# Optimization experiments

Hardware: AMD Instinct MI355X
Metric: run time of the kernel (lower is better)

The kernel has to match this reference:

```python
import jax, jax.numpy as jnp
import numpy as np

# ---- Cl(4,1) Cayley table (conformal GA: metric +,+,+,+,-) ----
_METRIC = (1.0, 1.0, 1.0, 1.0, -1.0)

def _reorder_sign(a, b):
    # sign from counting swaps to bring blade product to canonical order
    a >>= 1
    s = 0
    while a:
        s += bin(a & b).count("1")
        a >>= 1
    return -1.0 if (s & 1) else 1.0

def _build_cayley():
    C = np.zeros((32, 32, 32), dtype=np.float32)
    for a in range(32):
        for b in range(32):
            s = _reorder_sign(a, b)
            common = a & b
            for i in range(5):
                if (common >> i) & 1:
                    s *= _METRIC[i]
            C[a, b, a ^ b] += s
    return C

CAYLEY = _build_cayley()  # [32,32,32]; out_k = sum_ij C[i,j,k] x_i y_j

EPS = 1e-8

def normalize_cl41(x):
    n = jnp.sqrt(jnp.sum(x * x, axis=-1, keepdims=True))
    return x / (n + EPS)


def setup_inputs() -> dict:
    key = jax.random.key(0)
    k_x, k_wi, k_bi, k_wo, k_bo = jax.random.split(key, 5)
    B, S, D, H = 64, 2048, 6, 8
    x = jax.random.normal(k_x, (B, S, D), dtype=jnp.float32)
    W_in = jax.random.normal(k_wi, (D, H * 32), dtype=jnp.float32) * (1.0 / np.sqrt(D))
    b_in = jax.random.normal(k_bi, (H * 32,), dtype=jnp.float32) * 0.01
    W_out = jax.random.normal(k_wo, (H * 32, 32), dtype=jnp.float32) * (1.0 / np.sqrt(H * 32))
    b_out = jax.random.normal(k_bo, (32,), dtype=jnp.float32) * 0.01
    return {"x": x, "W_in": W_in, "b_in": b_in, "W_out": W_out, "b_out": b_out}


def reference(x, W_in, b_in, W_out, b_out):
    B, S, D = x.shape
    H = W_in.shape[1] // 32
    C = jnp.asarray(CAYLEY)
    # project inputs to per-channel multivectors: (B,S,H,32)
    u = (x @ W_in + b_in).reshape(B, S, H, 32)
    # initial rotor state: identity (scalar blade = 1)
    psi0 = jnp.zeros((B, H, 32), dtype=x.dtype).at[..., 0].set(1.0)

    def step(psi, u_t):  # u_t: (B,H,32)
        delta = normalize_cl41(u_t.at[..., 0].add(1.0))
        psi = normalize_cl41(jnp.einsum("bhi,bhj,ijk->bhk", delta, psi, C))
        return psi, psi

    _, psi_seq = jax.lax.scan(step, psi0, jnp.swapaxes(u, 0, 1))  # (S,B,H,32)
    out = normalize_cl41(psi_seq.reshape(S, B, H * 32) @ W_out + b_out)  # (S,B,32)
    return jnp.swapaxes(out, 0, 1)  # (B,S,32)
```

## Files before the change

kernel.cpp:

```cpp
#include <hip/hip_runtime.h>
#include <hip/hip_bf16.h>
#include <stdint.h>

#define BB 64
#define SS 2048
#define DD 6
#define HH 8
#define NCH 512
#define CHUNKS 256
#define LCH 8

typedef unsigned short ushort_t;
typedef __attribute__((ext_vector_type(8))) __bf16 bf16x8;
typedef __attribute__((ext_vector_type(4))) float f32x4;

struct SignTab { float s[32][32]; };

constexpr int popc5_c(unsigned v) {
    int c = 0;
    for (int i = 0; i < 5; ++i) c += (v >> i) & 1u;
    return c;
}

constexpr SignTab make_signs() {
    SignTab t{};
    for (int a = 0; a < 32; ++a) {
        for (int b = 0; b < 32; ++b) {
            int cnt = 0;
            unsigned aa = ((unsigned)a) >> 1;
            while (aa) { cnt += popc5_c(aa & (unsigned)b); aa >>= 1; }
            if ((a & b) & 16) cnt += 1;
            t.s[a][b] = (cnt & 1) ? -1.0f : 1.0f;
        }
    }
    return t;
}

constexpr SignTab SGN = make_signs();

__device__ __forceinline__ void gp_cl41(const float* __restrict__ a,
                                        const float* __restrict__ b,
                                        float* __restrict__ o) {
#pragma unroll
    for (int k = 0; k < 32; ++k) o[k] = 0.0f;
#pragma unroll
    for (int i = 0; i < 32; ++i) {
#pragma unroll
        for (int k = 0; k < 32; ++k) {
            o[k] = fmaf(SGN.s[i][i ^ k] * a[i], b[i ^ k], o[k]);
        }
    }
}

__device__ __forceinline__ float sumsq32(const float* v) {
    float n0 = 0.f, n1 = 0.f, n2 = 0.f, n3 = 0.f;
#pragma unroll
    for (int k = 0; k < 32; k += 4) {
        n0 = fmaf(v[k+0], v[k+0], n0);
        n1 = fmaf(v[k+1], v[k+1], n1);
        n2 = fmaf(v[k+2], v[k+2], n2);
        n3 = fmaf(v[k+3], v[k+3], n3);
    }
    return (n0 + n1) + (n2 + n3);
}

__device__ __forceinline__ float rsq(float n) {
    return __builtin_amdgcn_rsqf(n);
}

__device__ __forceinline__ uint32_t f2bf_rne(float f) {
    uint32_t u = __float_as_uint(f);
    return (u + 0x7FFFu + ((u >> 16) & 1u)) >> 16;
}

__device__ __forceinline__ void make_delta(const float4* __restrict__ sW,
                                           const float* __restrict__ x6,
                                           float* __restrict__ dl) {
#pragma unroll
    for (int j4 = 0; j4 < 8; ++j4) {
        float4 bv = sW[48 + j4];
        dl[4*j4+0] = bv.x; dl[4*j4+1] = bv.y; dl[4*j4+2] = bv.z; dl[4*j4+3] = bv.w;
    }
#pragma unroll
    for (int d = 0; d < 6; ++d) {
        float a = x6[d];
#pragma unroll
        for (int j4 = 0; j4 < 8; ++j4) {
            float4 w = sW[d * 8 + j4];
            dl[4*j4+0] = fmaf(a, w.x, dl[4*j4+0]);
            dl[4*j4+1] = fmaf(a, w.y, dl[4*j4+1]);
            dl[4*j4+2] = fmaf(a, w.z, dl[4*j4+2]);
            dl[4*j4+3] = fmaf(a, w.w, dl[4*j4+3]);
        }
    }
    dl[0] += 1.0f;
}

__global__ __launch_bounds__(256, 1) void k_scan(
        const float* __restrict__ x, const float* __restrict__ W_in,
        const float* __restrict__ b_in, float* __restrict__ Ebuf) {
    __shared__ float4 sW4[57];
    __shared__ float sT[CHUNKS][36];

    int chain = blockIdx.x;
    int b = chain >> 3, h = chain & 7;
    int c = threadIdx.x;

    if (c < 56) {
        float4 v;
        if (c < 48) {
            int d = c / 8, j4 = c % 8;
            const float* p = W_in + d * 256 + h * 32 + 4 * j4;
            v = make_float4(p[0], p[1], p[2], p[3]);
        } else {
            const float* p = b_in + h * 32 + 4 * (c - 48);
            v = make_float4(p[0], p[1], p[2], p[3]);
        }
        sW4[c] = v;
    }
    __syncthreads();

    const float* xrow = x + ((size_t)b * SS + (size_t)c * LCH) * DD;

    float P[32], O[32], dl[32];

    {
        float xv[12];
        const float4* xp = (const float4*)xrow;
#pragma unroll
        for (int m = 0; m < 3; ++m) {
            float4 t4 = xp[m];
            xv[4*m] = t4.x; xv[4*m+1] = t4.y; xv[4*m+2] = t4.z; xv[4*m+3] = t4.w;
        }
        make_delta(sW4, xv, O);
        make_delta(sW4, xv + 6, dl);
        gp_cl41(dl, O, P);
    }
#pragma unroll 1
    for (int pr = 1; pr < 4; ++pr) {
        float xv[12];
        const float4* xp = (const float4*)(xrow + 12 * pr);
#pragma unroll
        for (int m = 0; m < 3; ++m) {
            float4 t4 = xp[m];
            xv[4*m] = t4.x; xv[4*m+1] = t4.y; xv[4*m+2] = t4.z; xv[4*m+3] = t4.w;
        }
        make_delta(sW4, xv, dl);
        gp_cl41(dl, P, O);
        make_delta(sW4, xv + 6, dl);
        gp_cl41(dl, O, P);
    }

    float v[32];
    {
        float inv = rsq(sumsq32(P));
#pragma unroll
        for (int k = 0; k < 32; ++k) v[k] = P[k] * inv;
#pragma unroll
        for (int m = 0; m < 8; ++m)
            *(float4*)&sT[c][4*m] = make_float4(v[4*m], v[4*m+1], v[4*m+2], v[4*m+3]);
    }
    __syncthreads();

#pragma unroll 1
    for (int off = 1; off < CHUNKS; off <<= 1) {
        bool act = (c >= off);
        if (act) {
#pragma unroll
            for (int m = 0; m < 8; ++m) {
                float4 t4 = *(const float4*)&sT[c - off][4*m];
                O[4*m] = t4.x; O[4*m+1] = t4.y; O[4*m+2] = t4.z; O[4*m+3] = t4.w;
            }
        }
        __syncthreads();
        if (act) {
            gp_cl41(v, O, P);
            float inv = rsq(sumsq32(P));
#pragma unroll
            for (int k = 0; k < 32; ++k) v[k] = P[k] * inv;
#pragma unroll
            for (int m = 0; m < 8; ++m)
                *(float4*)&sT[c][4*m] = make_float4(v[4*m], v[4*m+1], v[4*m+2], v[4*m+3]);
        }
        __syncthreads();
    }

    float* dst = Ebuf + (size_t)chain * CHUNKS * 32;
    if (c == 0) {
        *(float4*)dst = make_float4(1.f, 0.f, 0.f, 0.f);
#pragma unroll
        for (int m = 1; m < 8; ++m) *(float4*)(dst + 4*m) = make_float4(0.f, 0.f, 0.f, 0.f);
    }
    if (c < CHUNKS - 1) {
        float* d2 = dst + (size_t)(c + 1) * 32;
#pragma unroll
        for (int m = 0; m < 8; ++m)
            *(float4*)(d2 + 4*m) = make_float4(v[4*m], v[4*m+1], v[4*m+2], v[4*m+3]);
    }
}

__global__ __launch_bounds__(64, 2) void k_chain_proj(
        const float* __restrict__ x, const float* __restrict__ W_in,
        const float* __restrict__ b_in, const float* __restrict__ Ebuf,
        const float* __restrict__ W_out, const float* __restrict__ b_out,
        float* __restrict__ out) {
    __shared__ float4 sW4[8][57];
    __shared__ float sX[384];
    __shared__ ushort_t psiT[16][264];

    int task = blockIdx.x;
    int b = task >> 5, grp = task & 31;
    int c0 = grp * 8;
    int lane = threadIdx.x;
    int cl = lane >> 3, h = lane & 7;
    int q = lane >> 4, n0 = lane & 15;

    for (int idx = lane; idx < 448; idx += 64) {
        int hh = idx / 56, r = idx % 56;
        float4 v;
        if (r < 48) {
            int d = r / 8, j4 = r % 8;
            const float* p = W_in + d * 256 + hh * 32 + 4 * j4;
            v = make_float4(p[0], p[1], p[2], p[3]);
        } else {
            const float* p = b_in + hh * 32 + 4 * (r - 48);
            v = make_float4(p[0], p[1], p[2], p[3]);
        }
        sW4[hh][r] = v;
    }

    {
        const float2* xp = (const float2*)(x + ((size_t)b * SS + (size_t)c0 * LCH) * DD);
        float2* sx2 = (float2*)sX;
#pragma unroll
        for (int m = 0; m < 3; ++m) sx2[lane * 3 + m] = xp[lane * 3 + m];
    }

    float p[32];
    {
        const float4* ep = (const float4*)(Ebuf +
                (((size_t)b * HH + h) * CHUNKS + (c0 + cl)) * 32);
#pragma unroll
        for (int m = 0; m < 8; ++m) {
            float4 t4 = ep[m];
            p[4*m] = t4.x; p[4*m+1] = t4.y; p[4*m+2] = t4.z; p[4*m+3] = t4.w;
        }
    }

    bf16x8 Bf[2][8];
#pragma unroll
    for (int nt = 0; nt < 2; ++nt)
#pragma unroll
        for (int kk = 0; kk < 8; ++kk) {
            union { ushort_t u[8]; bf16x8 v; } tmp;
#pragma unroll
            for (int j = 0; j < 8; ++j)
                tmp.u[j] = (ushort_t)f2bf_rne(W_out[(kk * 32 + q * 8 + j) * 32 + nt * 16 + n0]);
            Bf[nt][kk] = tmp.v;
        }
    float bn0 = b_out[n0], bn1 = b_out[16 + n0];

    __syncthreads();

#pragma unroll 1
    for (int pr = 0; pr < 4; ++pr) {
        float x0[6], x1[6];
#pragma unroll
        for (int d = 0; d < 6; ++d) {
            x0[d] = sX[(cl * 8 + 2 * pr) * 6 + d];
            x1[d] = sX[(cl * 8 + 2 * pr + 1) * 6 + d];
        }

        float dl[32], o[32];
        make_delta(sW4[h], x0, dl);
        gp_cl41(dl, p, o);
        {
            float inv = rsq(sumsq32(o));
            uint32_t pk[16];
#pragma unroll
            for (int m = 0; m < 16; ++m)
                pk[m] = f2bf_rne(o[2*m] * inv) | (f2bf_rne(o[2*m+1] * inv) << 16);
            uint4* dst = (uint4*)&psiT[cl * 2][h * 32];
#pragma unroll
            for (int m = 0; m < 4; ++m)
                dst[m] = make_uint4(pk[4*m], pk[4*m+1], pk[4*m+2], pk[4*m+3]);
        }
        make_delta(sW4[h], x1, dl);
        gp_cl41(dl, o, p);
        {
            float inv = rsq(sumsq32(p));
            uint32_t pk[16];
#pragma unroll
            for (int m = 0; m < 16; ++m)
                pk[m] = f2bf_rne(p[2*m] * inv) | (f2bf_rne(p[2*m+1] * inv) << 16);
            uint4* dst = (uint4*)&psiT[cl * 2 + 1][h * 32];
#pragma unroll
            for (int m = 0; m < 4; ++m)
                dst[m] = make_uint4(pk[4*m], pk[4*m+1], pk[4*m+2], pk[4*m+3]);
        }

        __syncthreads();

        f32x4 acc0 = {0.f, 0.f, 0.f, 0.f};
        f32x4 acc1 = {0.f, 0.f, 0.f, 0.f};
#pragma unroll
        for (int kk = 0; kk < 8; ++kk) {
            bf16x8 af = *(const bf16x8*)&psiT[n0][kk * 32 + q * 8];
            acc0 = __builtin_amdgcn_mfma_f32_16x16x32_bf16(af, Bf[0][kk], acc0, 0, 0, 0);
            acc1 = __builtin_amdgcn_mfma_f32_16x16x32_bf16(af, Bf[1][kk], acc1, 0, 0, 0);
        }

        float c0v[4], c1v[4], ssq[4];
#pragma unroll
        for (int i = 0; i < 4; ++i) {
            c0v[i] = acc0[i] + bn0;
            c1v[i] = acc1[i] + bn1;
            ssq[i] = c0v[i] * c0v[i] + c1v[i] * c1v[i];
        }
#pragma unroll
        for (int m = 1; m < 16; m <<= 1) {
#pragma unroll
            for (int i = 0; i < 4; ++i) ssq[i] += __shfl_xor(ssq[i], m);
        }
#pragma unroll
        for (int i = 0; i < 4; ++i) {
            float inv = rsq(ssq[i]);
            int mrow = q * 4 + i;
            int s = (c0 + (mrow >> 1)) * LCH + 2 * pr + (mrow & 1);
            size_t row = (size_t)b * SS + s;
            out[row * 32 + n0]      = c0v[i] * inv;
            out[row * 32 + 16 + n0] = c1v[i] * inv;
        }

        __syncthreads();
    }
}

extern "C" void kernel_launch(void* const* d_in, const int* in_sizes, int n_in,
                              void* d_out, int out_size, void* d_ws, size_t ws_size,
                              hipStream_t stream) {
    const float* x     = (const float*)d_in[0];
    const float* W_in  = (const float*)d_in[1];
    const float* b_in  = (const float*)d_in[2];
    const float* W_out = (const float*)d_in[3];
    const float* b_out = (const float*)d_in[4];
    float* out = (float*)d_out;

    float* Ebuf = (float*)d_ws;

    k_scan      <<<NCH,  256, 0, stream>>>(x, W_in, b_in, Ebuf);
    k_chain_proj<<<2048,  64, 0, stream>>>(x, W_in, b_in, Ebuf, W_out, b_out, out);
}
```

Baseline: 175.2 us.

## Replace Hillis-Steele chunk scan with tree-reduced scan and widen projection blocks

The per-chain chunk scan no longer runs an 8-level Hillis-Steele scan over 256 chunk products. It first combines pairs and quads into a 64-element level, scans that with a single wave over 6 levels, then expands the exclusive prefixes back to all 256 chunks. This cuts geometric products and block barriers. The projection kernel now packs four waves per block, stages W_out once into swizzled bf16 LDS instead of scattered global loads per lane, and uses an XOR-swizzled psiT layout to avoid bank conflicts. make_delta is fused to compute two step deltas at once. In exchange the scan uses more LDS, leaves three waves idle during the 64-wide scan, and changes the order of normalization.

Measured after the change: 192.6 us. 10.0% more time.

```diff
diff --git a/kernel.cpp b/kernel.cpp
--- a/kernel.cpp
+++ b/kernel.cpp
@@ -73,34 +73,68 @@
     return (u + 0x7FFFu + ((u >> 16) & 1u)) >> 16;
 }
 
-__device__ __forceinline__ void make_delta(const float4* __restrict__ sW,
-                                           const float* __restrict__ x6,
-                                           float* __restrict__ dl) {
+__device__ __forceinline__ void loadp(const float4* __restrict__ a, int stride,
+                                      int idx, float* __restrict__ v) {
+#pragma unroll
+    for (int m = 0; m < 8; ++m) {
+        float4 t = a[m * stride + idx];
+        v[4*m] = t.x; v[4*m+1] = t.y; v[4*m+2] = t.z; v[4*m+3] = t.w;
+    }
+}
+__device__ __forceinline__ void storep(float4* __restrict__ a, int stride,
+                                       int idx, const float* __restrict__ v) {
+#pragma unroll
+    for (int m = 0; m < 8; ++m)
+        a[m * stride + idx] = make_float4(v[4*m], v[4*m+1], v[4*m+2], v[4*m+3]);
+}
+
+__device__ __forceinline__ void make_delta2(const float4* __restrict__ sW,
+                                            const float* __restrict__ xv,
+                                            float* __restrict__ dl0,
+                                            float* __restrict__ dl1) {
 #pragma unroll
     for (int j4 = 0; j4 < 8; ++j4) {
         float4 bv = sW[48 + j4];
-        dl[4*j4+0] = bv.x; dl[4*j4+1] = bv.y; dl[4*j4+2] = bv.z; dl[4*j4+3] = bv.w;
+        dl0[4*j4+0] = bv.x; dl0[4*j4+1] = bv.y; dl0[4*j4+2] = bv.z; dl0[4*j4+3] = bv.w;
+        dl1[4*j4+0] = bv.x; dl1[4*j4+1] = bv.y; dl1[4*j4+2] = bv.z; dl1[4*j4+3] = bv.w;
     }
 #pragma unroll
     for (int d = 0; d < 6; ++d) {
-        float a = x6[d];
+        float a0 = xv[d], a1 = xv[6 + d];
 #pragma unroll
         for (int j4 = 0; j4 < 8; ++j4) {
             float4 w = sW[d * 8 + j4];
-            dl[4*j4+0] = fmaf(a, w.x, dl[4*j4+0]);
-            dl[4*j4+1] = fmaf(a, w.y, dl[4*j4+1]);
-            dl[4*j4+2] = fmaf(a, w.z, dl[4*j4+2]);
-            dl[4*j4+3] = fmaf(a, w.w, dl[4*j4+3]);
-        }
-    }
-    dl[0] += 1.0f;
+            dl0[4*j4+0] = fmaf(a0, w.x, dl0[4*j4+0]);
+            dl0[4*j4+1] = fmaf(a0, w.y, dl0[4*j4+1]);
+            dl0[4*j4+2] = fmaf(a0, w.z, dl0[4*j4+2]);
+            dl0[4*j4+3] = fmaf(a0, w.w, dl0[4*j4+3]);
+            dl1[4*j4+0] = fmaf(a1, w.x, dl1[4*j4+0]);
+            dl1[4*j4+1] = fmaf(a1, w.y, dl1[4*j4+1]);
+            dl1[4*j4+2] = fmaf(a1, w.z, dl1[4*j4+2]);
+            dl1[4*j4+3] = fmaf(a1, w.w, dl1[4*j4+3]);
+        }
+    }
+    dl0[0] += 1.0f;
+    dl1[0] += 1.0f;
+}
+
+__device__ __forceinline__ void loadx12(const float* __restrict__ xr, float* __restrict__ xv) {
+    const float4* xp = (const float4*)xr;
+#pragma unroll
+    for (int m = 0; m < 3; ++m) {
+        float4 t4 = xp[m];
+        xv[4*m] = t4.x; xv[4*m+1] = t4.y; xv[4*m+2] = t4.z; xv[4*m+3] = t4.w;
+    }
 }
 
 __global__ __launch_bounds__(256, 1) void k_scan(
         const float* __restrict__ x, const float* __restrict__ W_in,
         const float* __restrict__ b_in, float* __restrict__ Ebuf) {
     __shared__ float4 sW4[57];
-    __shared__ float sT[CHUNKS][36];
+    __shared__ float4 sTv[8 * CHUNKS];
+    __shared__ float4 sUv[8 * 128];
+    __shared__ float4 sGv[8 * 64];
+    __shared__ float4 sPv[8 * 64];
 
     int chain = blockIdx.x;
     int b = chain >> 3, h = chain & 7;
@@ -121,101 +155,132 @@
     __syncthreads();
 
     const float* xrow = x + ((size_t)b * SS + (size_t)c * LCH) * DD;
-
-    float P[32], O[32], dl[32];
-
+    float P[32], O[32];
     {
         float xv[12];
-        const float4* xp = (const float4*)xrow;
-#pragma unroll
-        for (int m = 0; m < 3; ++m) {
-            float4 t4 = xp[m];
-            xv[4*m] = t4.x; xv[4*m+1] = t4.y; xv[4*m+2] = t4.z; xv[4*m+3] = t4.w;
-        }
-        make_delta(sW4, xv, O);
-        make_delta(sW4, xv + 6, dl);
-        gp_cl41(dl, O, P);
+        loadx12(xrow, xv);
+        float dl0[32], dl1[32];
+        make_delta2(sW4, xv, dl0, dl1);
+        gp_cl41(dl1, dl0, P);
     }
 #pragma unroll 1
     for (int pr = 1; pr < 4; ++pr) {
         float xv[12];
-        const float4* xp = (const float4*)(xrow + 12 * pr);
-#pragma unroll
-        for (int m = 0; m < 3; ++m) {
-            float4 t4 = xp[m];
-            xv[4*m] = t4.x; xv[4*m+1] = t4.y; xv[4*m+2] = t4.z; xv[4*m+3] = t4.w;
-        }
-        make_delta(sW4, xv, dl);
-        gp_cl41(dl, P, O);
-        make_delta(sW4, xv + 6, dl);
-        gp_cl41(dl, O, P);
-    }
-
-    float v[32];
+        loadx12(xrow + 12 * pr, xv);
+        float dl0[32], dl1[32];
+        make_delta2(sW4, xv, dl0, dl1);
+        gp_cl41(dl0, P, O);
+        gp_cl41(dl1, O, P);
+    }
     {
         float inv = rsq(sumsq32(P));
 #pragma unroll
-        for (int k = 0; k < 32; ++k) v[k] = P[k] * inv;
+        for (int k = 0; k < 32; ++k) P[k] *= inv;
+        storep(sTv, CHUNKS, c, P);
+    }
+    __syncthreads();
+
+    int wave = c >> 6, lane = c & 63;
+    int w_act = (blockIdx.x ^ (blockIdx.x >> 8)) & 3;
+
+    if (c < 128) {
+        float A_[32], B_[32], U_[32];
+        loadp(sTv, CHUNKS, 2 * c + 1, A_);
+        loadp(sTv, CHUNKS, 2 * c,     B_);
+        gp_cl41(A_, B_, U_);
+        storep(sUv, 128, c, U_);
+    }
+    __syncthreads();
+
+    if (wave == w_act) {
+        float A_[32], B_[32], G_[32];
+        loadp(sUv, 128, 2 * lane + 1, A_);
+        loadp(sUv, 128, 2 * lane,     B_);
+        gp_cl41(A_, B_, G_);
+        storep(sGv, 64, lane, G_);
+    } else if (wave == (w_act ^ 2)) {
+        float A_[32], B_[32], P3_[32];
+        loadp(sTv, CHUNKS, 4 * lane + 2, A_);
+        loadp(sUv, 128, 2 * lane, B_);
+        gp_cl41(A_, B_, P3_);
+        storep(sPv, 64, lane, P3_);
+    }
+    __syncthreads();
+
+    {
+        bool act = (wave == w_act);
+        float gv[32];
+        if (act) loadp(sGv, 64, lane, gv);
+#pragma unroll 1
+        for (int off = 1; off < 64; off <<= 1) {
+            if (act && lane >= off) {
+                float w_[32], o_[32];
+                loadp(sGv, 64, lane - off, w_);
+                gp_cl41(gv, w_, o_);
+                float inv = rsq(sumsq32(o_));
+#pragma unroll
+                for (int k = 0; k < 32; ++k) gv[k] = o_[k] * inv;
+                storep(sGv, 64, lane, gv);
+            }
+            __syncthreads();
+        }
+    }
+
+    {
+        int g = c >> 2, r = c & 3;
+        float EG[32], E_[32];
+        if (g == 0) {
+#pragma unroll
+            for (int k = 0; k < 32; ++k) EG[k] = (k == 0) ? 1.f : 0.f;
+        } else {
+            loadp(sGv, 64, g - 1, EG);
+        }
+        if (r == 0) {
+#pragma unroll
+            for (int k = 0; k < 32; ++k) E_[k] = EG[k];
+        } else {
+            float L[32];
+            if (r == 1)      loadp(sTv, CHUNKS, c - 1, L);
+            else if (r == 2) loadp(sUv, 128, (c - 2) >> 1, L);
+            else             loadp(sPv, 64, g, L);
+            gp_cl41(L, EG, E_);
+        }
+        float inv = rsq(sumsq32(E_));
+        float4* dst = (float4*)(Ebuf + ((size_t)chain * CHUNKS + c) * 32);
 #pragma unroll
         for (int m = 0; m < 8; ++m)
-            *(float4*)&sT[c][4*m] = make_float4(v[4*m], v[4*m+1], v[4*m+2], v[4*m+3]);
-    }
-    __syncthreads();
-
-#pragma unroll 1
-    for (int off = 1; off < CHUNKS; off <<= 1) {
-        bool act = (c >= off);
-        if (act) {
-#pragma unroll
-            for (int m = 0; m < 8; ++m) {
-                float4 t4 = *(const float4*)&sT[c - off][4*m];
-                O[4*m] = t4.x; O[4*m+1] = t4.y; O[4*m+2] = t4.z; O[4*m+3] = t4.w;
-            }
-        }
-        __syncthreads();
-        if (act) {
-            gp_cl41(v, O, P);
-            float inv = rsq(sumsq32(P));
-#pragma unroll
-            for (int k = 0; k < 32; ++k) v[k] = P[k] * inv;
-#pragma unroll
-            for (int m = 0; m < 8; ++m)
-                *(float4*)&sT[c][4*m] = make_float4(v[4*m], v[4*m+1], v[4*m+2], v[4*m+3]);
-        }
-        __syncthreads();
-    }
-
-    float* dst = Ebuf + (size_t)chain * CHUNKS * 32;
-    if (c == 0) {
-        *(float4*)dst = make_float4(1.f, 0.f, 0.f, 0.f);
-#pragma unroll
-        for (int m = 1; m < 8; ++m) *(float4*)(dst + 4*m) = make_float4(0.f, 0.f, 0.f, 0.f);
-    }
-    if (c < CHUNKS - 1) {
-        float* d2 = dst + (size_t)(c + 1) * 32;
-#pragma unroll
-        for (int m = 0; m < 8; ++m)
-            *(float4*)(d2 + 4*m) = make_float4(v[4*m], v[4*m+1], v[4*m+2], v[4*m+3]);
-    }
-}
-
-__global__ __launch_bounds__(64, 2) void k_chain_proj(
+            dst[m] = make_float4(E_[4*m] * inv, E_[4*m+1] * inv,
+                                 E_[4*m+2] * inv, E_[4*m+3] * inv);
+    }
+}
+
+__global__ __launch_bounds__(256, 1) void k_chain_proj(
         const float* __restrict__ x, const float* __restrict__ W_in,
         const float* __restrict__ b_in, const float* __restrict__ Ebuf,
         const float* __restrict__ W_out, const float* __restrict__ b_out,
         float* __restrict__ out) {
     __shared__ float4 sW4[8][57];
-    __shared__ float sX[384];
-    __shared__ ushort_t psiT[16][264];
-
-    int task = blockIdx.x;
-    int b = task >> 5, grp = task & 31;
+    __shared__ float sX[1536];
+    __shared__ ushort_t Wt[32 * 256];
+    __shared__ ushort_t psiT[4 * 16 * 256];
+
+    int tid = threadIdx.x;
+    int wv = tid >> 6, lane = tid & 63;
+    int b = blockIdx.x >> 3, gq = blockIdx.x & 7;
+    int grp = gq * 4 + wv;
     int c0 = grp * 8;
-    int lane = threadIdx.x;
     int cl = lane >> 3, h = lane & 7;
     int q = lane >> 4, n0 = lane & 15;
 
-    for (int idx = lane; idx < 448; idx += 64) {
+    float4 pv[8];
+    {
+        const float4* ep = (const float4*)(Ebuf +
+                (((size_t)b * HH + h) * CHUNKS + (c0 + cl)) * 32);
+#pragma unroll
+        for (int m = 0; m < 8; ++m) pv[m] = ep[m];
+    }
+
+    for (int idx = tid; idx < 448; idx += 256) {
         int hh = idx / 56, r = idx % 56;
         float4 v;
         if (r < 48) {
@@ -230,84 +295,101 @@
     }
 
     {
-        const float2* xp = (const float2*)(x + ((size_t)b * SS + (size_t)c0 * LCH) * DD);
-        float2* sx2 = (float2*)sX;
-#pragma unroll
-        for (int m = 0; m < 3; ++m) sx2[lane * 3 + m] = xp[lane * 3 + m];
-    }
+        const float4* xp = (const float4*)(x + ((size_t)b * SS + (size_t)gq * 256) * DD);
+        float4* sx4 = (float4*)sX;
+        for (int idx = tid; idx < 384; idx += 256) sx4[idx] = xp[idx];
+    }
+
+    for (int idx = tid; idx < 2048; idx += 256) {
+        int k = idx >> 3, n4 = (idx & 7) << 2;
+        float4 w4 = ((const float4*)W_out)[idx];
+        ushort_t vals[4] = { (ushort_t)f2bf_rne(w4.x), (ushort_t)f2bf_rne(w4.y),
+                             (ushort_t)f2bf_rne(w4.z), (ushort_t)f2bf_rne(w4.w) };
+#pragma unroll
+        for (int j = 0; j < 4; ++j) {
+            int n = n4 + j;
+            uint32_t off = (uint32_t)(n * 512 + 2 * k) ^ (uint32_t)((n & 7) << 4);
+            *(ushort_t*)((char*)Wt + off) = vals[j];
+        }
+    }
+    __syncthreads();
 
     float p[32];
-    {
-        const float4* ep = (const float4*)(Ebuf +
-                (((size_t)b * HH + h) * CHUNKS + (c0 + cl)) * 32);
-#pragma unroll
-        for (int m = 0; m < 8; ++m) {
-            float4 t4 = ep[m];
-            p[4*m] = t4.x; p[4*m+1] = t4.y; p[4*m+2] = t4.z; p[4*m+3] = t4.w;
-        }
+#pragma unroll
+    for (int m = 0; m < 8; ++m) {
+        p[4*m] = pv[m].x; p[4*m+1] = pv[m].y; p[4*m+2] = pv[m].z; p[4*m+3] = pv[m].w;
     }
 
     bf16x8 Bf[2][8];
 #pragma unroll
-    for (int nt = 0; nt < 2; ++nt)
-#pragma unroll
-        for (int kk = 0; kk < 8; ++kk) {
-            union { ushort_t u[8]; bf16x8 v; } tmp;
-#pragma unroll
-            for (int j = 0; j < 8; ++j)
-                tmp.u[j] = (ushort_t)f2bf_rne(W_out[(kk * 32 + q * 8 + j) * 32 + nt * 16 + n0]);
-            Bf[nt][kk] = tmp.v;
-        }
+    for (int nt = 0; nt < 2; ++nt) {
+        int n = nt * 16 + n0;
+        uint32_t rb = (uint32_t)(n * 512);
+        uint32_t sw = (uint32_t)((n & 7) << 4);
+#pragma unroll
+        for (int kk = 0; kk < 8; ++kk)
+            Bf[nt][kk] = *(const bf16x8*)((const char*)Wt + ((rb + kk * 64 + q * 16) ^ sw));
+    }
     float bn0 = b_out[n0], bn1 = b_out[16 + n0];
 
-    __syncthreads();
+    ushort_t* myT = psiT + wv * 16 * 256;
 
 #pragma unroll 1
     for (int pr = 0; pr < 4; ++pr) {
-        float x0[6], x1[6];
-#pragma unroll
-        for (int d = 0; d < 6; ++d) {
-            x0[d] = sX[(cl * 8 + 2 * pr) * 6 + d];
-            x1[d] = sX[(cl * 8 + 2 * pr + 1) * 6 + d];
-        }
-
-        float dl[32], o[32];
-        make_delta(sW4[h], x0, dl);
-        gp_cl41(dl, p, o);
+        float xv[12];
+        {
+            const float* xr = sX + (wv * 64 + cl * 8 + 2 * pr) * 6;
+#pragma unroll
+            for (int d = 0; d < 12; ++d) xv[d] = xr[d];
+        }
+
+        float dl0[32], dl1[32], o[32];
+        make_delta2(sW4[h], xv, dl0, dl1);
+
+        gp_cl41(dl0, p, o);
         {
             float inv = rsq(sumsq32(o));
+            int row = cl * 2;
+            uint32_t rb = (uint32_t)(row * 512 + h * 64);
+            uint32_t sw = (uint32_t)((row & 7) << 4);
             uint32_t pk[16];
 #pragma unroll
             for (int m = 0; m < 16; ++m)
                 pk[m] = f2bf_rne(o[2*m] * inv) | (f2bf_rne(o[2*m+1] * inv) << 16);
-            uint4* dst = (uint4*)&psiT[cl * 2][h * 32];
 #pragma unroll
             for (int m = 0; m < 4; ++m)
-                dst[m] = make_uint4(pk[4*m], pk[4*m+1], pk[4*m+2], pk[4*m+3]);
-        }
-        make_delta(sW4[h], x1, dl);
-        gp_cl41(dl, o, p);
+                *(uint4*)((char*)myT + ((rb + 16 * m) ^ sw)) =
+                    make_uint4(pk[4*m], pk[4*m+1], pk[4*m+2], pk[4*m+3]);
+        }
+        gp_cl41(dl1, o, p);
         {
             float inv = rsq(sumsq32(p));
+            int row = cl * 2 + 1;
+            uint32_t rb = (uint32_t)(row * 512 + h * 64);
+            uint32_t sw = (uint32_t)((row & 7) << 4);
             uint32_t pk[16];
 #pragma unroll
             for (int m = 0; m < 16; ++m)
                 pk[m] = f2bf_rne(p[2*m] * inv) | (f2bf_rne(p[2*m+1] * inv) << 16);
-            uint4* dst = (uint4*)&psiT[cl * 2 + 1][h * 32];
 #pragma unroll
             for (int m = 0; m < 4; ++m)
-                dst[m] = make_uint4(pk[4*m], pk[4*m+1], pk[4*m+2], pk[4*m+3]);
+                *(uint4*)((char*)myT + ((rb + 16 * m) ^ sw)) =
+                    make_uint4(pk[4*m], pk[4*m+1], pk[4*m+2], pk[4*m+3]);
         }
 
         __syncthreads();
 
         f32x4 acc0 = {0.f, 0.f, 0.f, 0.f};
         f32x4 acc1 = {0.f, 0.f, 0.f, 0.f};
-#pragma unroll
-        for (int kk = 0; kk < 8; ++kk) {
-            bf16x8 af = *(const bf16x8*)&psiT[n0][kk * 32 + q * 8];
-            acc0 = __builtin_amdgcn_mfma_f32_16x16x32_bf16(af, Bf[0][kk], acc0, 0, 0, 0);
-            acc1 = __builtin_amdgcn_mfma_f32_16x16x32_bf16(af, Bf[1][kk], acc1, 0, 0, 0);
+        {
+            uint32_t rb = (uint32_t)(n0 * 512);
+            uint32_t sw = (uint32_t)((n0 & 7) << 4);
+#pragma unroll
+            for (int kk = 0; kk < 8; ++kk) {
+                bf16x8 af = *(const bf16x8*)((const char*)myT + ((rb + kk * 64 + q * 16) ^ sw));
+                acc0 = __builtin_amdgcn_mfma_f32_16x16x32_bf16(af, Bf[0][kk], acc0, 0, 0, 0);
+                acc1 = __builtin_amdgcn_mfma_f32_16x16x32_bf16(af, Bf[1][kk], acc1, 0, 0, 0);
+            }
         }
 
         float c0v[4], c1v[4], ssq[4];
@@ -348,6 +430,6 @@
 
     float* Ebuf = (float*)d_ws;
 
-    k_scan      <<<NCH,  256, 0, stream>>>(x, W_in, b_in, Ebuf);
-    k_chain_proj<<<2048,  64, 0, stream>>>(x, W_in, b_in, Ebuf, W_out, b_out, out);
-}
+    k_scan      <<<NCH, 256, 0, stream>>>(x, W_in, b_in, Ebuf);
+    k_chain_proj<<<NCH, 256, 0, stream>>>(x, W_in, b_in, Ebuf, W_out, b_out, out);
+}
```
